# Performance work log

Measured on AMD Instinct MI355X. Metric: run time of the kernel, lower is better.

The kernel has to match this reference:

```python
import jax, jax.numpy as jnp
import numpy as np

B, L, D = 4, 2048, 2048
H, KVH, HD = 16, 4, 128          # num_heads, num_kv_heads, head_dim = D // H
M = 16                           # mem_tokens
BASE = 10000.0
EPS = 1.1920929e-07              # torch F.rms_norm default eps = fp32 machine eps


def _rms_norm(x):
    # normalize over last dim, no learned weight (matches F.rms_norm(x, (hd,)))
    return x * jax.lax.rsqrt(jnp.mean(x * x, axis=-1, keepdims=True) + EPS)


def _apply_rotary(x, cos, sin):
    # x: [B, h, T, HD]; cos/sin: [1, 1, T, HD//2]
    half = x.shape[-1] // 2
    x1, x2 = x[..., :half], x[..., half:]
    return jnp.concatenate([x1 * cos + x2 * sin, -x1 * sin + x2 * cos], axis=-1)


def setup_inputs() -> dict:
    key = jax.random.key(0)
    k0, k1, k2, k3, k4 = jax.random.split(key, 5)
    kv_dim = KVH * HD
    s = 0.02
    return {
        "x": jax.random.normal(k0, (B, L, D), dtype=jnp.float32),
        "Wq": jax.random.normal(k1, (D, D), dtype=jnp.float32) * s,
        "Wk": jax.random.normal(k2, (kv_dim, D), dtype=jnp.float32) * s,
        "Wv": jax.random.normal(k3, (kv_dim, D), dtype=jnp.float32) * s,
        "Wproj": jax.random.normal(k4, (D, D), dtype=jnp.float32) * s,
        "q_gain": jnp.full((H,), 1.0, dtype=jnp.float32),
    }


def reference(x, Wq, Wk, Wv, Wproj, q_gain):
    Bx, Lx, Dx = x.shape
    # QKV projections (Linear: x @ W.T), split into heads -> [B, h, L, HD]
    q = (x @ Wq.T).reshape(Bx, Lx, H, HD).transpose(0, 2, 1, 3)
    k = (x @ Wk.T).reshape(Bx, Lx, KVH, HD).transpose(0, 2, 1, 3)
    v = (x @ Wv.T).reshape(Bx, Lx, KVH, HD).transpose(0, 2, 1, 3)
    # QK RMSNorm
    q = _rms_norm(q)
    k = _rms_norm(k)
    # RoPE on the non-memory tokens only
    T = Lx - M
    inv_freq = 1.0 / BASE ** (jnp.arange(0, HD, 2, dtype=jnp.float32) / HD)
    freqs = jnp.outer(jnp.arange(T, dtype=jnp.float32), inv_freq)  # [T, HD//2]
    cos = jnp.cos(freqs)[None, None]
    sin = jnp.sin(freqs)[None, None]
    q = jnp.concatenate([q[:, :, :M], _apply_rotary(q[:, :, M:], cos, sin)], axis=2)
    k = jnp.concatenate([k[:, :, :M], _apply_rotary(k[:, :, M:], cos, sin)], axis=2)
    # per-head gain on q
    q = q * q_gain[None, :, None, None]
    # GQA attention: group q heads by kv head (matches repeat_interleave ordering)
    rep = H // KVH
    qg = q.reshape(Bx, KVH, rep, Lx, HD)
    scale = 1.0 / np.sqrt(HD).astype(np.float32)
    scores = jnp.einsum('bgrqd,bgkd->bgrqk', qg, k) * scale  # [B, KVH, rep, L, L]
    causal = jnp.tril(jnp.ones((Lx, Lx), dtype=bool))
    scores = jnp.where(causal, scores, -jnp.inf)
    p = jax.nn.softmax(scores, axis=-1)
    y = jnp.einsum('bgrqk,bgkd->bgrqd', p, v)                # [B, KVH, rep, L, HD]
    y = y.reshape(Bx, H, Lx, HD).transpose(0, 2, 1, 3).reshape(Bx, Lx, Dx)
    return y @ Wproj.T
```

## Files before the change

### kernel.cpp

```cpp
#include <hip/hip_runtime.h>
#include <stdint.h>

typedef unsigned short u16;
typedef short s8v __attribute__((ext_vector_type(8)));
typedef float f4v __attribute__((ext_vector_type(4)));
typedef float f16v __attribute__((ext_vector_type(16)));

typedef __attribute__((address_space(1))) char gchar;
typedef __attribute__((address_space(3))) char lchar;

static __device__ __forceinline__ u16 f2bf(float f) {
  uint32_t x = __float_as_uint(f);
  x += 0x7fffu + ((x >> 16) & 1u);
  return (u16)(x >> 16);
}
static __device__ __forceinline__ float bf2f(u16 u) {
  return __uint_as_float(((uint32_t)u) << 16);
}
static __device__ __forceinline__ void gload_lds16(const void* g, void* l) {
  __builtin_amdgcn_global_load_lds((gchar*)(uintptr_t)g,
                                   (lchar*)(uint32_t)(uintptr_t)l, 16, 0, 0);
}

__global__ __launch_bounds__(256) void cvt_bf16(const float4* __restrict__ src,
                                                uint2* __restrict__ dst, int n4) {
  int i = blockIdx.x * 256 + threadIdx.x;
  int st = gridDim.x * 256;
  for (; i < n4; i += st) {
    float4 v = src[i];
    uint2 o;
    o.x = (uint32_t)f2bf(v.x) | ((uint32_t)f2bf(v.y) << 16);
    o.y = (uint32_t)f2bf(v.z) | ((uint32_t)f2bf(v.w) << 16);
    dst[i] = o;
  }
}

__global__ __launch_bounds__(256) void cvt_bf16_w(const float4* __restrict__ s0,
                                                  const float4* __restrict__ s1,
                                                  const float4* __restrict__ s2,
                                                  const float4* __restrict__ s3,
                                                  uint2* __restrict__ dst) {
  int i = blockIdx.x * 256 + threadIdx.x;
  int st = gridDim.x * 256;
  for (; i < 2621440; i += st) {
    const float4* s;
    int off;
    if (i < 1048576)      { s = s0; off = i; }
    else if (i < 1310720) { s = s1; off = i - 1048576; }
    else if (i < 1572864) { s = s2; off = i - 1310720; }
    else                  { s = s3; off = i - 1572864; }
    float4 v = s[off];
    uint2 o;
    o.x = (uint32_t)f2bf(v.x) | ((uint32_t)f2bf(v.y) << 16);
    o.y = (uint32_t)f2bf(v.z) | ((uint32_t)f2bf(v.w) << 16);
    dst[i] = o;
  }
}

__global__ __launch_bounds__(256) void rope_table(float* __restrict__ tc,
                                                  float* __restrict__ ts) {
  int i = blockIdx.x * 256 + threadIdx.x;
  if (i >= 2032 * 64) return;
  int t = i >> 6, f = i & 63;
  float invf = 1.0f / powf(10000.0f, (float)f * (1.0f / 64.0f));
  float ang = (float)t * invf;
  float s, c;
  sincosf(ang, &s, &c);
  tc[i] = c;
  ts[i] = s;
}

template <int BN, int OUT>
__global__ __launch_bounds__(512, 2) void gemm_nt(
    const u16* __restrict__ A, const u16* __restrict__ Wt,
    u16* __restrict__ Oa, u16* __restrict__ Ob2, float* __restrict__ OF) {
  constexpr int MI = (BN == 256) ? 8 : 4;
  constexpr int BLOADS = (BN == 256) ? 2 : 1;
  __shared__ u16 lA[2][2][256 * 32];
  __shared__ u16 lB[2][2][BN * 32];
  const int tid = threadIdx.x;
  const int lane = tid & 63, wid = tid >> 6;
  const int wr = (BN == 256) ? (wid >> 2) : (wid >> 1);
  const int wc = (BN == 256) ? (wid & 3) : (wid & 1);
  const int l15 = lane & 15, l4 = lane >> 4;

  const int bid = blockIdx.x;
  const int swz = (bid & 7) * 32 + (bid >> 3);
  const int bn = swz >> 5, bm = swz & 31;
  const int m0 = bm * 256;
  const int n0r = bn * BN;

  auto stage_part = [&](int kt, int bs, int ks) {
    const int kb = kt * 64 + ks * 32;
#pragma unroll
    for (int c = 0; c < 2; ++c) {
      int cidx = tid + c * 512;
      int r = cidx >> 2, q = cidx & 3;
      int cc = q ^ ((r >> 2) & 3);
      gload_lds16(A + (size_t)(m0 + r) * 2048 + kb + cc * 8,
                  &lA[bs][ks][cidx * 8]);
    }
#pragma unroll
    for (int c = 0; c < BLOADS; ++c) {
      int cidx = tid + c * 512;
      int r = cidx >> 2, q = cidx & 3;
      int cc = q ^ ((r >> 2) & 3);
      gload_lds16(Wt + (size_t)(n0r + r) * 2048 + kb + cc * 8,
                  &lB[bs][ks][cidx * 8]);
    }
  };
  auto roff = [&](int fr, int c) {
    return (fr * 4 + (c ^ ((fr >> 2) & 3))) * 8;
  };

  const f4v Z4 = {0.f, 0.f, 0.f, 0.f};
  f4v acc[MI][4];
#pragma unroll
  for (int i = 0; i < MI; i++)
#pragma unroll
    for (int j = 0; j < 4; j++) acc[i][j] = Z4;

  stage_part(0, 0, 0); stage_part(0, 0, 1);
  stage_part(1, 1, 0); stage_part(1, 1, 1);

  const int NT = 32;
  for (int t = 0; t < NT; ++t) {
    const int bs = t & 1;
    if (t + 1 < NT) {
      if constexpr (BN == 256) asm volatile("s_waitcnt vmcnt(8)" ::: "memory");
      else                     asm volatile("s_waitcnt vmcnt(6)" ::: "memory");
    } else {
      asm volatile("s_waitcnt vmcnt(0)" ::: "memory");
    }
    asm volatile("s_barrier" ::: "memory");
    const bool pf = (t + 2 < NT);
#pragma unroll
    for (int ks = 0; ks < 2; ++ks) {
      s8v afrg[MI], bfrg[4];
#pragma unroll
      for (int i = 0; i < MI; ++i)
        afrg[i] = *(const s8v*)&lA[bs][ks][roff(wr * (MI * 16) + i * 16 + l15, l4)];
#pragma unroll
      for (int j = 0; j < 4; ++j)
        bfrg[j] = *(const s8v*)&lB[bs][ks][roff(wc * 64 + j * 16 + l15, l4)];
      asm volatile("s_waitcnt lgkmcnt(0)" ::: "memory");
      __builtin_amdgcn_sched_barrier(0);
      asm volatile("s_barrier" ::: "memory");
      if (pf) stage_part(t + 2, bs, ks);
      __builtin_amdgcn_s_setprio(1);
#pragma unroll
      for (int i = 0; i < MI; ++i)
#pragma unroll
        for (int j = 0; j < 4; ++j)
          acc[i][j] = __builtin_amdgcn_mfma_f32_16x16x32_bf16(afrg[i], bfrg[j], acc[i][j], 0, 0, 0);
      __builtin_amdgcn_s_setprio(0);
    }
  }

  const int colg = bn * BN + wc * 64;
  if constexpr (OUT == 0) {
    const int hh = colg >> 7, d0 = colg & 127;
#pragma unroll
    for (int i = 0; i < MI; i++)
#pragma unroll
      for (int r = 0; r < 4; r++) {
        int m = m0 + wr * (MI * 16) + i * 16 + l4 * 4 + r;
        int b = m >> 11, l = m & 2047;
        size_t base = ((size_t)(b * 16 + hh) * 2048 + l) * 128 + d0;
#pragma unroll
        for (int j = 0; j < 4; j++)
          Oa[base + j * 16 + l15] = f2bf(acc[i][j][r]);
      }
  } else if constexpr (OUT == 1) {
    u16* Ob = (colg < 512) ? Oa : Ob2;
    const int hh = (colg & 511) >> 7, d0 = colg & 127;
#pragma unroll
    for (int i = 0; i < MI; i++)
#pragma unroll
      for (int r = 0; r < 4; r++) {
        int m = m0 + wr * (MI * 16) + i * 16 + l4 * 4 + r;
        int b = m >> 11, l = m & 2047;
        size_t base = ((size_t)(b * 4 + hh) * 2048 + l) * 128 + d0;
#pragma unroll
        for (int j = 0; j < 4; j++)
          Ob[base + j * 16 + l15] = f2bf(acc[i][j][r]);
      }
  } else {
#pragma unroll
    for (int i = 0; i < MI; i++)
#pragma unroll
      for (int r = 0; r < 4; r++) {
        int m = m0 + wr * (MI * 16) + i * 16 + l4 * 4 + r;
#pragma unroll
        for (int j = 0; j < 4; j++)
          OF[(size_t)m * 2048 + colg + j * 16 + l15] = acc[i][j][r];
      }
  }
}

__global__ __launch_bounds__(256) void norm_rope_k(u16* __restrict__ buf,
                                                   const float* __restrict__ tc,
                                                   const float* __restrict__ ts) {
  const int lane = threadIdx.x & 63;
  const int gw = blockIdx.x * 4 + (threadIdx.x >> 6);
  const int nw = gridDim.x * 4;
  for (int row = gw; row < 32768; row += nw) {
    int l = row & 2047;
    u16* p = buf + (size_t)row * 128;
    float x1 = bf2f(p[lane]);
    float x2 = bf2f(p[lane + 64]);
    float ss = x1 * x1 + x2 * x2;
#pragma unroll
    for (int off = 32; off > 0; off >>= 1) ss += __shfl_xor(ss, off, 64);
    float r = rsqrtf(ss * (1.0f / 128.0f) + 1.1920929e-07f);
    x1 *= r; x2 *= r;
    if (l >= 16) {
      int t = l - 16;
      float c = tc[t * 64 + lane], s = ts[t * 64 + lane];
      float o1 = x1 * c + x2 * s;
      float o2 = -x1 * s + x2 * c;
      x1 = o1; x2 = o2;
    }
    p[lane] = f2bf(x1);
    p[lane + 64] = f2bf(x2);
  }
}

__global__ __launch_bounds__(256) void transpose_v(const u16* __restrict__ v,
                                                   u16* __restrict__ vt) {
  __shared__ u16 t[64][64];
  const int l0 = blockIdx.x * 64, d0 = blockIdx.y * 64, bg = blockIdx.z;
  const int tid = threadIdx.x;
#pragma unroll
  for (int it = 0; it < 2; ++it) {
    int lin = it * 256 + tid;
    int r = lin >> 3, cb = lin & 7;
    s8v val = *(const s8v*)&v[((bg * 2048 + l0 + r) * 128) + d0 + cb * 8];
    *(s8v*)&t[r][(cb ^ (r & 7)) * 8] = val;
  }
  __syncthreads();
#pragma unroll
  for (int it = 0; it < 2; ++it) {
    int lin = it * 256 + tid;
    int r2 = lin >> 3, c2 = (lin & 7) * 8;
    s8v o;
#pragma unroll
    for (int j = 0; j < 8; ++j) {
      int rr = c2 + j, cc = r2;
      o[j] = (short)t[rr][(cc & 7) + 8 * ((cc >> 3) ^ (rr & 7))];
    }
    *(s8v*)&vt[((bg * 128 + d0 + r2) * 2048) + l0 + c2] = o;
  }
}

__global__ __launch_bounds__(512, 2) void attn(const u16* __restrict__ q,
                                               const u16* __restrict__ k,
                                               const u16* __restrict__ vt,
                                               u16* __restrict__ y,
                                               const float* __restrict__ qg,
                                               const float* __restrict__ tc,
                                               const float* __restrict__ ts) {
  __shared__ u16 lK[2][64 * 128];
  __shared__ u16 lVT[2][128 * 64];
  const int tid = threadIdx.x;
  const int lane = tid & 63, wid = tid >> 6;
  const int l31 = lane & 31, hi = lane >> 5;

  const int bid = (int)blockIdx.x;
  const int bg = (bid & 7) * 2 + (bid >> 7);
  const int pairi = (bid >> 3) & 15;
  const int b = bg >> 2, g = bg & 3;
  const int h = g * 4 + (wid & 3);
  const int se = wid >> 2;

  const u16* qh = q + (size_t)(b * 16 + h) * 2048 * 128;
  const u16* kb0 = k + (size_t)(b * 4 + g) * 2048 * 128;
  const u16* vtb0 = vt + (size_t)(b * 4 + g) * 128 * 2048;
  const float gscale = qg[h] * (0.08838834764831845f * 1.4426950408889634f);

  auto stage = [&](int t, int bufsel) {
    const int kv0 = t * 64;
#pragma unroll
    for (int it = 0; it < 2; ++it) {
      int lin = it * 512 + tid;
      int kj = lin >> 4, s = lin & 15;
      gload_lds16(kb0 + (size_t)(kv0 + kj) * 128 + ((s ^ (kj & 7)) * 8),
                  &lK[bufsel][lin * 8]);
    }
#pragma unroll
    for (int it = 0; it < 2; ++it) {
      int lin = it * 512 + tid;
      int d = lin >> 3, s = lin & 7;
      gload_lds16(vtb0 + (size_t)d * 2048 + kv0 + ((s ^ (d & 7)) * 8),
                  &lVT[bufsel][lin * 8]);
    }
  };

  for (int ph = 0; ph < 2; ++ph) {
    const int qt = ph ? (31 - pairi) : pairi;
    const int q0 = qt * 64;
    const int nt = qt + 1;
    const int pos = q0 + 32 * se + l31;

    s8v qf[8];
    {
      const u16* qp = qh + (size_t)pos * 128 + hi * 8;
      s8v qr[8];
#pragma unroll
      for (int ks = 0; ks < 8; ++ks) qr[ks] = *(const s8v*)&qp[ks * 16];
      float ssum = 0.f;
#pragma unroll
      for (int ks = 0; ks < 8; ++ks)
#pragma unroll
        for (int j = 0; j < 8; ++j) {
          float v = bf2f((u16)qr[ks][j]);
          ssum += v * v;
        }
      ssum += __shfl_xor(ssum, 32, 64);
      const float rn = rsqrtf(ssum * (1.0f / 128.0f) + 1.1920929e-07f) * gscale;
      const bool rot = (pos >= 16);
      const int tt = pos - 16;
#pragma unroll
      for (int ks = 0; ks < 4; ++ks) {
        float cv[8], sv[8];
        if (rot) {
          const float* cp = &tc[tt * 64 + ks * 16 + hi * 8];
          const float* sp = &ts[tt * 64 + ks * 16 + hi * 8];
          *(float4*)&cv[0] = *(const float4*)cp;
          *(float4*)&cv[4] = *(const float4*)(cp + 4);
          *(float4*)&sv[0] = *(const float4*)sp;
          *(float4*)&sv[4] = *(const float4*)(sp + 4);
        }
        uint32_t wlo[4], whi[4];
#pragma unroll
        for (int j2 = 0; j2 < 4; ++j2) {
          float o1[2], o2[2];
#pragma unroll
          for (int e = 0; e < 2; ++e) {
            const int j = j2 * 2 + e;
            float x1 = bf2f((u16)qr[ks][j]);
            float x2 = bf2f((u16)qr[ks + 4][j]);
            float a = x1, bb = x2;
            if (rot) { a = x1 * cv[j] + x2 * sv[j]; bb = x2 * cv[j] - x1 * sv[j]; }
            o1[e] = a * rn;
            o2[e] = bb * rn;
          }
          asm("v_cvt_pk_bf16_f32 %0, %1, %2" : "=v"(wlo[j2]) : "v"(o1[0]), "v"(o1[1]));
          asm("v_cvt_pk_bf16_f32 %0, %1, %2" : "=v"(whi[j2]) : "v"(o2[0]), "v"(o2[1]));
        }
        union { uint32_t u[4]; s8v v; } ua, ub;
        ua.u[0] = wlo[0]; ua.u[1] = wlo[1]; ua.u[2] = wlo[2]; ua.u[3] = wlo[3];
        ub.u[0] = whi[0]; ub.u[1] = whi[1]; ub.u[2] = whi[2]; ub.u[3] = whi[3];
        qf[ks] = ua.v;
        qf[ks + 4] = ub.v;
      }
    }

    f16v yacc[4];
#pragma unroll
    for (int j = 0; j < 4; ++j)
#pragma unroll
      for (int r = 0; r < 16; ++r) yacc[j][r] = 0.f;
    float mrow = -1e30f, lrow = 0.f;

    stage(0, 0);
    __syncthreads();

    for (int t = 0; t < nt; ++t) {
      const int cur = t & 1;
      if (t + 1 < nt) stage(t + 1, cur ^ 1);
      const int kv0 = t * 64;

      f16v s0a, s1a;
#pragma unroll
      for (int r = 0; r < 16; ++r) { s0a[r] = 0.f; s1a[r] = 0.f; }
      __builtin_amdgcn_s_setprio(1);
#pragma unroll
      for (int ks = 0; ks < 8; ++ks) {
        const int slot = (2 * ks + hi) ^ (l31 & 7);
        s8v kf0 = *(const s8v*)&lK[cur][(l31)*128 + slot * 8];
        s8v kf1 = *(const s8v*)&lK[cur][(32 + l31) * 128 + slot * 8];
        s0a = __builtin_amdgcn_mfma_f32_32x32x16_bf16(kf0, qf[ks], s0a, 0, 0, 0);
        s1a = __builtin_amdgcn_mfma_f32_32x32x16_bf16(kf1, qf[ks], s1a, 0, 0, 0);
      }
      __builtin_amdgcn_s_setprio(0);

      const bool last = (t == nt - 1);
      float p0[16], p1[16];
      float pmax = -1e30f;
#pragma unroll
      for (int r = 0; r < 16; ++r) {
        const int kvloc = (r & 3) + 8 * (r >> 2) + 4 * hi;
        float v0 = s0a[r];
        float v1 = s1a[r];
        if (last) {
          if (kv0 + kvloc > pos) v0 = -1e30f;
          if (kv0 + 32 + kvloc > pos) v1 = -1e30f;
        }
        p0[r] = v0; p1[r] = v1;
        pmax = fmaxf(pmax, fmaxf(v0, v1));
      }
      pmax = fmaxf(pmax, __shfl_xor(pmax, 32, 64));

      if (!__all(pmax - mrow <= 11.541560327111707f)) {
        float mnew = fmaxf(mrow, pmax);
        float corr = __builtin_amdgcn_exp2f(mrow - mnew);
#pragma unroll
        for (int r = 0; r < 16; ++r) {
          const int qloc = (r & 3) + 8 * (r >> 2) + 4 * hi;
          float cb = __shfl(corr, qloc, 64);
          yacc[0][r] *= cb; yacc[1][r] *= cb; yacc[2][r] *= cb; yacc[3][r] *= cb;
        }
        lrow *= corr;
        mrow = mnew;
      }

      float ps = 0.f;
#pragma unroll
      for (int r = 0; r < 16; ++r) {
        float e0 = __builtin_amdgcn_exp2f(p0[r] - mrow);
        float e1 = __builtin_amdgcn_exp2f(p1[r] - mrow);
        p0[r] = e0; p1[r] = e1;
        ps += e0 + e1;
      }
      ps += __shfl_xor(ps, 32, 64);
      lrow += ps;

      __builtin_amdgcn_s_setprio(1);
#pragma unroll
      for (int ks = 0; ks < 4; ++ks) {
        const float* pc = (ks < 2) ? p0 : p1;
        const int rb = 8 * (ks & 1);
        uint32_t A0, A1, B0, B1;
        asm("v_cvt_pk_bf16_f32 %0, %1, %2" : "=v"(A0) : "v"(pc[rb + 0]), "v"(pc[rb + 1]));
        asm("v_cvt_pk_bf16_f32 %0, %1, %2" : "=v"(A1) : "v"(pc[rb + 2]), "v"(pc[rb + 3]));
        asm("v_cvt_pk_bf16_f32 %0, %1, %2" : "=v"(B0) : "v"(pc[rb + 4]), "v"(pc[rb + 5]));
        asm("v_cvt_pk_bf16_f32 %0, %1, %2" : "=v"(B1) : "v"(pc[rb + 6]), "v"(pc[rb + 7]));
        asm("v_permlane32_swap_b32 %0, %1" : "+v"(A0), "+v"(B0));
        asm("v_permlane32_swap_b32 %0, %1" : "+v"(A1), "+v"(B1));
        union { uint32_t u[4]; s8v v; } uu;
        uu.u[0] = A0; uu.u[1] = A1; uu.u[2] = B0; uu.u[3] = B1;
#pragma unroll
        for (int jd = 0; jd < 4; ++jd) {
          const int rowd = 32 * jd + l31;
          const int slot = (2 * ks + hi) ^ (l31 & 7);
          s8v vf = *(const s8v*)&lVT[cur][rowd * 64 + slot * 8];
          yacc[jd] = __builtin_amdgcn_mfma_f32_32x32x16_bf16(uu.v, vf, yacc[jd], 0, 0, 0);
        }
      }
      __builtin_amdgcn_s_setprio(0);
      __syncthreads();
    }

    float inv = 1.0f / lrow;
#pragma unroll
    for (int r = 0; r < 16; ++r) {
      const int qloc = (r & 3) + 8 * (r >> 2) + 4 * hi;
      float ib = __shfl(inv, qloc, 64);
      const int qrow = q0 + 32 * se + qloc;
      size_t base = ((size_t)(b * 2048 + qrow)) * 2048 + h * 128 + l31;
#pragma unroll
      for (int jd = 0; jd < 4; ++jd)
        y[base + 32 * jd] = f2bf(yacc[jd][r] * ib);
    }
  }
}

extern "C" void kernel_launch(void* const* d_in, const int* in_sizes, int n_in,
                              void* d_out, int out_size, void* d_ws, size_t ws_size,
                              hipStream_t stream) {
  const float* x  = (const float*)d_in[0];
  const float* Wq = (const float*)d_in[1];
  const float* Wk = (const float*)d_in[2];
  const float* Wv = (const float*)d_in[3];
  const float* Wp = (const float*)d_in[4];
  const float* qg = (const float*)d_in[5];
  float* out = (float*)d_out;

  char* ws = (char*)d_ws;
  size_t off = 0;
  auto alloc = [&](size_t bytes) {
    void* p = ws + off;
    off += (bytes + 255) & ~(size_t)255;
    return p;
  };
  u16* x_bf  = (u16*)alloc((size_t)8192 * 2048 * 2);
  u16* wq_bf = (u16*)alloc((size_t)2048 * 2048 * 2);
  u16* wk_bf = (u16*)alloc((size_t)512 * 2048 * 2);
  u16* wv_bf = (u16*)alloc((size_t)512 * 2048 * 2);
  u16* wp_bf = (u16*)alloc((size_t)2048 * 2048 * 2);
  u16* q_bf  = (u16*)alloc((size_t)4 * 16 * 2048 * 128 * 2);
  u16* k_bf  = (u16*)alloc((size_t)4 * 4 * 2048 * 128 * 2);
  u16* v_bf  = (u16*)alloc((size_t)4 * 4 * 2048 * 128 * 2);
  float* tab = (float*)alloc((size_t)2032 * 64 * 2 * 4);
  u16* y_bf  = x_bf;
  u16* vt_bf = wq_bf;

  cvt_bf16<<<2048, 256, 0, stream>>>((const float4*)x, (uint2*)x_bf, 8192 * 2048 / 4);
  cvt_bf16_w<<<1024, 256, 0, stream>>>((const float4*)Wq, (const float4*)Wk,
                                       (const float4*)Wv, (const float4*)Wp,
                                       (uint2*)wq_bf);
  rope_table<<<(2032 * 64 + 255) / 256, 256, 0, stream>>>(tab, tab + 2032 * 64);

  gemm_nt<256, 0><<<dim3(256), 512, 0, stream>>>(x_bf, wq_bf, q_bf, nullptr, nullptr);
  gemm_nt<128, 1><<<dim3(256), 512, 0, stream>>>(x_bf, wk_bf, k_bf, v_bf, nullptr);
  norm_rope_k<<<256, 256, 0, stream>>>(k_bf, tab, tab + 2032 * 64);
  transpose_v<<<dim3(32, 2, 16), 256, 0, stream>>>(v_bf, vt_bf);
  attn<<<dim3(256), 512, 0, stream>>>(q_bf, k_bf, vt_bf, y_bf, qg,
                                      tab, tab + 2032 * 64);
  gemm_nt<256, 2><<<dim3(256), 512, 0, stream>>>(y_bf, wp_bf, nullptr, nullptr, out);
}
```

Baseline: 353.7 us.

## Restructure 256x256 GEMMs into four-phase quarter-tile pipeline with finer prefetch interleave

Replaces the 256x256 tile GEMM used for the Q and output projections with a new kernel. It stages A and B in 64-wide K slices split into halves with XOR-swizzled LDS layout, and computes the tile in four quadrant phases. Global-to-LDS prefetches for the next tiles are interleaved between the phases, so memory traffic overlaps MFMA work at a finer grain and fewer fragment registers are live at once. The KV GEMM keeps the old scheme as its own kernel. The cost is many more barriers per iteration and a more fragile vmcnt accounting.

After: 344.0 us. -2.7%, faster.

```diff
diff --git a/kernel.cpp b/kernel.cpp
--- a/kernel.cpp
+++ b/kernel.cpp
@@ -70,25 +70,198 @@
   ts[i] = s;
 }
 
-template <int BN, int OUT>
-__global__ __launch_bounds__(512, 2) void gemm_nt(
+template <int OUT>
+__global__ __launch_bounds__(512, 2) void gemm8(
     const u16* __restrict__ A, const u16* __restrict__ Wt,
-    u16* __restrict__ Oa, u16* __restrict__ Ob2, float* __restrict__ OF) {
-  constexpr int MI = (BN == 256) ? 8 : 4;
-  constexpr int BLOADS = (BN == 256) ? 2 : 1;
-  __shared__ u16 lA[2][2][256 * 32];
-  __shared__ u16 lB[2][2][BN * 32];
+    u16* __restrict__ Oa, float* __restrict__ OF) {
+  __shared__ u16 lA[2][2][128 * 64];
+  __shared__ u16 lB[2][2][128 * 64];
   const int tid = threadIdx.x;
   const int lane = tid & 63, wid = tid >> 6;
-  const int wr = (BN == 256) ? (wid >> 2) : (wid >> 1);
-  const int wc = (BN == 256) ? (wid & 3) : (wid & 1);
+  const int wr = wid >> 2, wc = wid & 3;
   const int l15 = lane & 15, l4 = lane >> 4;
 
   const int bid = blockIdx.x;
   const int swz = (bid & 7) * 32 + (bid >> 3);
   const int bn = swz >> 5, bm = swz & 31;
   const int m0 = bm * 256;
-  const int n0r = bn * BN;
+  const int n0r = bn * 256;
+
+  auto stageA = [&](int kt, int bs, int mh) {
+    const int kb = kt * 64;
+#pragma unroll
+    for (int c = 0; c < 2; ++c) {
+      int cidx = tid + c * 512;
+      int rr = cidx >> 3, pc = cidx & 7;
+      int grow = mh * 64 + (rr & 63) + ((rr >> 6) << 7);
+      int kc = pc ^ (rr & 7);
+      gload_lds16(A + (size_t)(m0 + grow) * 2048 + kb + kc * 8,
+                  &lA[bs][mh][cidx * 8]);
+    }
+  };
+  auto stageB = [&](int kt, int bs, int nh) {
+    const int kb = kt * 64;
+#pragma unroll
+    for (int c = 0; c < 2; ++c) {
+      int cidx = tid + c * 512;
+      int rr = cidx >> 3, pc = cidx & 7;
+      int gn = ((rr >> 5) << 6) + nh * 32 + (rr & 31);
+      int kc = pc ^ (rr & 7);
+      gload_lds16(Wt + (size_t)(n0r + gn) * 2048 + kb + kc * 8,
+                  &lB[bs][nh][cidx * 8]);
+    }
+  };
+  auto readA = [&](int bs, int mh, int i, int ks) {
+    int rr = wr * 64 + i * 16 + l15;
+    return *(const s8v*)&lA[bs][mh][rr * 64 + (((ks * 4 + l4) ^ (rr & 7)) << 3)];
+  };
+  auto readB = [&](int bs, int nh, int j, int ks) {
+    int rr = wc * 32 + j * 16 + l15;
+    return *(const s8v*)&lB[bs][nh][rr * 64 + (((ks * 4 + l4) ^ (rr & 7)) << 3)];
+  };
+
+  const f4v Z4 = {0.f, 0.f, 0.f, 0.f};
+  f4v acc[8][4];
+#pragma unroll
+  for (int i = 0; i < 8; i++)
+#pragma unroll
+    for (int j = 0; j < 4; j++) acc[i][j] = Z4;
+
+  stageA(0, 0, 0); stageA(0, 0, 1); stageB(0, 0, 0); stageB(0, 0, 1);
+  stageA(1, 1, 0); stageA(1, 1, 1); stageB(1, 1, 0);
+  asm volatile("s_waitcnt vmcnt(6)" ::: "memory");
+  asm volatile("s_barrier" ::: "memory");
+
+  const int NT = 32;
+  for (int t = 0; t < NT; ++t) {
+    const int bs = t & 1, nbs = bs ^ 1;
+    s8v a[4][2], b[2][2];
+#pragma unroll
+    for (int i = 0; i < 4; ++i)
+#pragma unroll
+      for (int ks = 0; ks < 2; ++ks) a[i][ks] = readA(bs, 0, i, ks);
+#pragma unroll
+    for (int j = 0; j < 2; ++j)
+#pragma unroll
+      for (int ks = 0; ks < 2; ++ks) b[j][ks] = readB(bs, 0, j, ks);
+    if (t + 1 < NT) stageB(t + 1, nbs, 1);
+    asm volatile("s_barrier" ::: "memory");
+    asm volatile("s_waitcnt lgkmcnt(0)" ::: "memory");
+    __builtin_amdgcn_sched_barrier(0);
+    __builtin_amdgcn_s_setprio(1);
+#pragma unroll
+    for (int i = 0; i < 4; ++i)
+#pragma unroll
+      for (int j = 0; j < 2; ++j)
+#pragma unroll
+        for (int ks = 0; ks < 2; ++ks)
+          acc[i][j] = __builtin_amdgcn_mfma_f32_16x16x32_bf16(a[i][ks], b[j][ks], acc[i][j], 0, 0, 0);
+    __builtin_amdgcn_s_setprio(0);
+    asm volatile("s_barrier" ::: "memory");
+#pragma unroll
+    for (int j = 0; j < 2; ++j)
+#pragma unroll
+      for (int ks = 0; ks < 2; ++ks) b[j][ks] = readB(bs, 1, j, ks);
+    if (t + 2 < NT) stageA(t + 2, bs, 0);
+    asm volatile("s_barrier" ::: "memory");
+    asm volatile("s_waitcnt lgkmcnt(0)" ::: "memory");
+    __builtin_amdgcn_sched_barrier(0);
+    __builtin_amdgcn_s_setprio(1);
+#pragma unroll
+    for (int i = 0; i < 4; ++i)
+#pragma unroll
+      for (int j = 0; j < 2; ++j)
+#pragma unroll
+        for (int ks = 0; ks < 2; ++ks)
+          acc[i][2 + j] = __builtin_amdgcn_mfma_f32_16x16x32_bf16(a[i][ks], b[j][ks], acc[i][2 + j], 0, 0, 0);
+    __builtin_amdgcn_s_setprio(0);
+    asm volatile("s_barrier" ::: "memory");
+#pragma unroll
+    for (int i = 0; i < 4; ++i)
+#pragma unroll
+      for (int ks = 0; ks < 2; ++ks) a[i][ks] = readA(bs, 1, i, ks);
+#pragma unroll
+    for (int j = 0; j < 2; ++j)
+#pragma unroll
+      for (int ks = 0; ks < 2; ++ks) b[j][ks] = readB(bs, 0, j, ks);
+    asm volatile("s_barrier" ::: "memory");
+    asm volatile("s_waitcnt lgkmcnt(0)" ::: "memory");
+    __builtin_amdgcn_sched_barrier(0);
+    __builtin_amdgcn_s_setprio(1);
+#pragma unroll
+    for (int i = 0; i < 4; ++i)
+#pragma unroll
+      for (int j = 0; j < 2; ++j)
+#pragma unroll
+        for (int ks = 0; ks < 2; ++ks)
+          acc[4 + i][j] = __builtin_amdgcn_mfma_f32_16x16x32_bf16(a[i][ks], b[j][ks], acc[4 + i][j], 0, 0, 0);
+    __builtin_amdgcn_s_setprio(0);
+    asm volatile("s_barrier" ::: "memory");
+#pragma unroll
+    for (int j = 0; j < 2; ++j)
+#pragma unroll
+      for (int ks = 0; ks < 2; ++ks) b[j][ks] = readB(bs, 1, j, ks);
+    if (t + 2 < NT) { stageA(t + 2, bs, 1); stageB(t + 2, bs, 0); }
+    asm volatile("s_barrier" ::: "memory");
+    asm volatile("s_waitcnt lgkmcnt(0)" ::: "memory");
+    __builtin_amdgcn_sched_barrier(0);
+    __builtin_amdgcn_s_setprio(1);
+#pragma unroll
+    for (int i = 0; i < 4; ++i)
+#pragma unroll
+      for (int j = 0; j < 2; ++j)
+#pragma unroll
+        for (int ks = 0; ks < 2; ++ks)
+          acc[4 + i][2 + j] = __builtin_amdgcn_mfma_f32_16x16x32_bf16(a[i][ks], b[j][ks], acc[4 + i][2 + j], 0, 0, 0);
+    __builtin_amdgcn_s_setprio(0);
+    if (t + 2 < NT)      asm volatile("s_waitcnt vmcnt(6)" ::: "memory");
+    else if (t + 1 < NT) asm volatile("s_waitcnt vmcnt(0)" ::: "memory");
+    asm volatile("s_barrier" ::: "memory");
+  }
+
+  const int colg0 = bn * 256 + wc * 64;
+  if constexpr (OUT == 0) {
+    const int hh = colg0 >> 7, d0 = colg0 & 127;
+#pragma unroll
+    for (int i = 0; i < 8; i++)
+#pragma unroll
+      for (int r = 0; r < 4; r++) {
+        int m = m0 + wr * 128 + (i >> 2) * 64 + (i & 3) * 16 + l4 * 4 + r;
+        int b2 = m >> 11, l = m & 2047;
+        size_t base = ((size_t)(b2 * 16 + hh) * 2048 + l) * 128 + d0;
+#pragma unroll
+        for (int j = 0; j < 4; j++)
+          Oa[base + (j >> 1) * 32 + (j & 1) * 16 + l15] = f2bf(acc[i][j][r]);
+      }
+  } else {
+#pragma unroll
+    for (int i = 0; i < 8; i++)
+#pragma unroll
+      for (int r = 0; r < 4; r++) {
+        int m = m0 + wr * 128 + (i >> 2) * 64 + (i & 3) * 16 + l4 * 4 + r;
+#pragma unroll
+        for (int j = 0; j < 4; j++)
+          OF[(size_t)m * 2048 + colg0 + (j >> 1) * 32 + (j & 1) * 16 + l15] = acc[i][j][r];
+      }
+  }
+}
+
+__global__ __launch_bounds__(512, 2) void gemm_kv(
+    const u16* __restrict__ A, const u16* __restrict__ Wt,
+    u16* __restrict__ Oa, u16* __restrict__ Ob2) {
+  constexpr int MI = 4;
+  __shared__ u16 lA[2][2][256 * 32];
+  __shared__ u16 lB[2][2][128 * 32];
+  const int tid = threadIdx.x;
+  const int lane = tid & 63, wid = tid >> 6;
+  const int wr = wid >> 1, wc = wid & 1;
+  const int l15 = lane & 15, l4 = lane >> 4;
+
+  const int bid = blockIdx.x;
+  const int swz = (bid & 7) * 32 + (bid >> 3);
+  const int bn = swz >> 5, bm = swz & 31;
+  const int m0 = bm * 256;
+  const int n0r = bn * 128;
 
   auto stage_part = [&](int kt, int bs, int ks) {
     const int kb = kt * 64 + ks * 32;
@@ -100,9 +273,8 @@
       gload_lds16(A + (size_t)(m0 + r) * 2048 + kb + cc * 8,
                   &lA[bs][ks][cidx * 8]);
     }
-#pragma unroll
-    for (int c = 0; c < BLOADS; ++c) {
-      int cidx = tid + c * 512;
+    {
+      int cidx = tid;
       int r = cidx >> 2, q = cidx & 3;
       int cc = q ^ ((r >> 2) & 3);
       gload_lds16(Wt + (size_t)(n0r + r) * 2048 + kb + cc * 8,
@@ -126,12 +298,8 @@
   const int NT = 32;
   for (int t = 0; t < NT; ++t) {
     const int bs = t & 1;
-    if (t + 1 < NT) {
-      if constexpr (BN == 256) asm volatile("s_waitcnt vmcnt(8)" ::: "memory");
-      else                     asm volatile("s_waitcnt vmcnt(6)" ::: "memory");
-    } else {
-      asm volatile("s_waitcnt vmcnt(0)" ::: "memory");
-    }
+    if (t + 1 < NT) asm volatile("s_waitcnt vmcnt(6)" ::: "memory");
+    else            asm volatile("s_waitcnt vmcnt(0)" ::: "memory");
     asm volatile("s_barrier" ::: "memory");
     const bool pf = (t + 2 < NT);
 #pragma unroll
@@ -157,45 +325,20 @@
     }
   }
 
-  const int colg = bn * BN + wc * 64;
-  if constexpr (OUT == 0) {
-    const int hh = colg >> 7, d0 = colg & 127;
-#pragma unroll
-    for (int i = 0; i < MI; i++)
-#pragma unroll
-      for (int r = 0; r < 4; r++) {
-        int m = m0 + wr * (MI * 16) + i * 16 + l4 * 4 + r;
-        int b = m >> 11, l = m & 2047;
-        size_t base = ((size_t)(b * 16 + hh) * 2048 + l) * 128 + d0;
-#pragma unroll
-        for (int j = 0; j < 4; j++)
-          Oa[base + j * 16 + l15] = f2bf(acc[i][j][r]);
-      }
-  } else if constexpr (OUT == 1) {
-    u16* Ob = (colg < 512) ? Oa : Ob2;
-    const int hh = (colg & 511) >> 7, d0 = colg & 127;
-#pragma unroll
-    for (int i = 0; i < MI; i++)
-#pragma unroll
-      for (int r = 0; r < 4; r++) {
-        int m = m0 + wr * (MI * 16) + i * 16 + l4 * 4 + r;
-        int b = m >> 11, l = m & 2047;
-        size_t base = ((size_t)(b * 4 + hh) * 2048 + l) * 128 + d0;
-#pragma unroll
-        for (int j = 0; j < 4; j++)
-          Ob[base + j * 16 + l15] = f2bf(acc[i][j][r]);
-      }
-  } else {
-#pragma unroll
-    for (int i = 0; i < MI; i++)
-#pragma unroll
-      for (int r = 0; r < 4; r++) {
-        int m = m0 + wr * (MI * 16) + i * 16 + l4 * 4 + r;
-#pragma unroll
-        for (int j = 0; j < 4; j++)
-          OF[(size_t)m * 2048 + colg + j * 16 + l15] = acc[i][j][r];
-      }
-  }
+  const int colg = bn * 128 + wc * 64;
+  u16* Ob = (colg < 512) ? Oa : Ob2;
+  const int hh = (colg & 511) >> 7, d0 = colg & 127;
+#pragma unroll
+  for (int i = 0; i < MI; i++)
+#pragma unroll
+    for (int r = 0; r < 4; r++) {
+      int m = m0 + wr * (MI * 16) + i * 16 + l4 * 4 + r;
+      int b = m >> 11, l = m & 2047;
+      size_t base = ((size_t)(b * 4 + hh) * 2048 + l) * 128 + d0;
+#pragma unroll
+      for (int j = 0; j < 4; j++)
+        Ob[base + j * 16 + l15] = f2bf(acc[i][j][r]);
+    }
 }
 
 __global__ __launch_bounds__(256) void norm_rope_k(u16* __restrict__ buf,
@@ -502,11 +645,11 @@
                                        (uint2*)wq_bf);
   rope_table<<<(2032 * 64 + 255) / 256, 256, 0, stream>>>(tab, tab + 2032 * 64);
 
-  gemm_nt<256, 0><<<dim3(256), 512, 0, stream>>>(x_bf, wq_bf, q_bf, nullptr, nullptr);
-  gemm_nt<128, 1><<<dim3(256), 512, 0, stream>>>(x_bf, wk_bf, k_bf, v_bf, nullptr);
+  gemm8<0><<<dim3(256), 512, 0, stream>>>(x_bf, wq_bf, q_bf, nullptr);
+  gemm_kv<<<dim3(256), 512, 0, stream>>>(x_bf, wk_bf, k_bf, v_bf);
   norm_rope_k<<<256, 256, 0, stream>>>(k_bf, tab, tab + 2032 * 64);
   transpose_v<<<dim3(32, 2, 16), 256, 0, stream>>>(v_bf, vt_bf);
   attn<<<dim3(256), 512, 0, stream>>>(q_bf, k_bf, vt_bf, y_bf, qg,
                                       tab, tab + 2032 * 64);
-  gemm_nt<256, 2><<<dim3(256), 512, 0, stream>>>(y_bf, wp_bf, nullptr, nullptr, out);
-}
+  gemm8<2><<<dim3(256), 512, 0, stream>>>(y_bf, wp_bf, nullptr, out);
+}
```
